# Performance work log

Measured on AMD Instinct MI355X. Metric: run time of the kernel, lower is better.

Reference implementation:

```python
import jax, jax.numpy as jnp
import numpy as np

D_K = 64


def setup_inputs() -> dict:
    key = jax.random.key(0)
    kq, kk, kv = jax.random.split(key, 3)
    B, H, S, D = 4, 16, 2048, 64
    return {
        "query": jax.random.normal(kq, (B, H, S, D), dtype=jnp.float32),
        "key": jax.random.normal(kk, (B, H, S, D), dtype=jnp.float32),
        "value": jax.random.normal(kv, (B, H, S, D), dtype=jnp.float32),
        "to_mask": 1,
    }


def reference(query, key, value, to_mask):
    # QK^T / sqrt(d_k): [B,H,S,S]
    scores = jnp.einsum("bhqd,bhkd->bhqk", query, key) / jnp.sqrt(
        jnp.asarray(D_K, dtype=query.dtype)
    )
    if to_mask:
        S = scores.shape[-1]
        # upper-triangular (strictly above diagonal) gets large negative bias
        causal = jnp.triu(jnp.ones((S, S), dtype=scores.dtype), k=1)
        scores = scores + causal[None, None, :, :] * jnp.asarray(-1e19, scores.dtype)
    attn = jax.nn.softmax(scores, axis=-1)
    return jnp.einsum("bhqk,bhkd->bhqd", attn, value)
```

## Files before the change

kernel.cpp:

```cpp
#include <hip/hip_runtime.h>
#include <math.h>

#define S_LEN 2048
#define D_HEAD 64
#define NT 32
#define BM 128
#define BN 64
#define TILE_HALFS 4096
#define PSTRIDE 72
#define QSCALE (0.125f * 1.44269504088896340736f)

typedef _Float16 f16;
typedef f16 f16x4 __attribute__((ext_vector_type(4)));
typedef f16 f16x8 __attribute__((ext_vector_type(8)));
typedef float f32x4 __attribute__((ext_vector_type(4)));

#define ASYNC16(g, l)                                                          \
    __builtin_amdgcn_global_load_lds(                                          \
        (const __attribute__((address_space(1))) void*)(g),                    \
        (__attribute__((address_space(3))) void*)(l), 16, 0, 0)

__global__ __launch_bounds__(256)
void prepass_kernel(const float* __restrict__ K, const float* __restrict__ V,
                    f16* __restrict__ Kw, f16* __restrict__ Vw) {
    const int kt = blockIdx.x, bh = blockIdx.y, tid = threadIdx.x;
    const int t = tid >> 6, lane = tid & 63, c = lane & 15, quad = lane >> 4;
    const size_t gbase = (size_t)bh * S_LEN * D_HEAD + (size_t)kt * BN * D_HEAD;
    const size_t tb = ((size_t)bh * NT + kt) * TILE_HALFS;

    __shared__ float Kt_s[64][65];
    __shared__ float Vt_s[64][65];

    float4 kv[4], vv[4];
    #pragma unroll
    for (int i = 0; i < 4; ++i) {
        const int fi = tid + i * 256;
        const int row = fi >> 4, d0 = (fi & 15) * 4;
        kv[i] = *(const float4*)(K + gbase + row * 64 + d0);
        vv[i] = *(const float4*)(V + gbase + row * 64 + d0);
    }
    #pragma unroll
    for (int i = 0; i < 4; ++i) {
        const int fi = tid + i * 256;
        const int row = fi >> 4, d0 = (fi & 15) * 4;
        Kt_s[row][d0 + 0] = kv[i].x; Kt_s[row][d0 + 1] = kv[i].y;
        Kt_s[row][d0 + 2] = kv[i].z; Kt_s[row][d0 + 3] = kv[i].w;
        Vt_s[row][d0 + 0] = vv[i].x; Vt_s[row][d0 + 1] = vv[i].y;
        Vt_s[row][d0 + 2] = vv[i].z; Vt_s[row][d0 + 3] = vv[i].w;
    }
    __syncthreads();

    #pragma unroll
    for (int ch = 0; ch < 2; ++ch) {
        const float* src = &Kt_s[t * 16 + c][ch * 32 + quad * 8];
        f16 h[8];
        #pragma unroll
        for (int j = 0; j < 8; ++j) h[j] = (f16)src[j];
        *(f16x8*)&Kw[tb + (size_t)((t * 2 + ch) * 64 + lane) * 8] = *(f16x8*)h;
    }
    #pragma unroll
    for (int ch = 0; ch < 2; ++ch) {
        f16 h[8];
        #pragma unroll
        for (int j = 0; j < 8; ++j)
            h[j] = (f16)Vt_s[ch * 32 + quad * 8 + j][t * 16 + c];
        *(f16x8*)&Vw[tb + (size_t)((t * 2 + ch) * 64 + lane) * 8] = *(f16x8*)h;
    }
}

__global__ __launch_bounds__(256, 3)
void fa_fwd_kernel(const float* __restrict__ Q, const f16* __restrict__ Kw,
                   const f16* __restrict__ Vw, const int* __restrict__ to_mask,
                   float* __restrict__ O) {
    const int qt   = (int)gridDim.x - 1 - (int)blockIdx.x;
    const int bh   = blockIdx.y;
    const int tid  = threadIdx.x;
    const int wave = tid >> 6;
    const int lane = tid & 63;
    const int c    = lane & 15;
    const int quad = lane >> 4;
    const int i0   = qt * BM;
    const int wrow0 = i0 + wave * 32;

    const int mask_on = to_mask[0];
    const int kt_end  = mask_on ? (2 * qt + 1) : (NT - 1);

    __shared__ __align__(16) f16 KV[2][2][TILE_HALFS];
    __shared__ __align__(16) f16 Ps[BM][PSTRIDE];

    const size_t base  = (size_t)bh * S_LEN * D_HEAD;
    const size_t tbase = (size_t)bh * NT * TILE_HALFS;

    f16x8 aq[2][2];
    #pragma unroll
    for (int set = 0; set < 2; ++set) {
        const float* qp = Q + base + (size_t)(wrow0 + set * 16 + c) * D_HEAD + quad * 8;
        #pragma unroll
        for (int ch = 0; ch < 2; ++ch) {
            const float4 a = *(const float4*)(qp + ch * 32);
            const float4 b = *(const float4*)(qp + ch * 32 + 4);
            aq[set][ch][0] = (f16)(a.x * QSCALE); aq[set][ch][1] = (f16)(a.y * QSCALE);
            aq[set][ch][2] = (f16)(a.z * QSCALE); aq[set][ch][3] = (f16)(a.w * QSCALE);
            aq[set][ch][4] = (f16)(b.x * QSCALE); aq[set][ch][5] = (f16)(b.y * QSCALE);
            aq[set][ch][6] = (f16)(b.z * QSCALE); aq[set][ch][7] = (f16)(b.w * QSCALE);
        }
    }

    f32x4 o[2][4];
    f32x4 accl[2];
    #pragma unroll
    for (int set = 0; set < 2; ++set) {
        accl[set] = (f32x4){0.f, 0.f, 0.f, 0.f};
        #pragma unroll
        for (int nt = 0; nt < 4; ++nt) o[set][nt] = (f32x4){0.f, 0.f, 0.f, 0.f};
    }

    const f16 one1 = (f16)1.0f;
    const f16x8 ones = {one1, one1, one1, one1, one1, one1, one1, one1};

    #pragma unroll
    for (int i = 0; i < 2; ++i) {
        const int s = wave * 2 + i;
        ASYNC16(Kw + tbase + s * 512 + lane * 8, &KV[0][0][s * 512]);
        ASYNC16(Vw + tbase + s * 512 + lane * 8, &KV[0][1][s * 512]);
    }

    for (int kt = 0; kt <= kt_end; ++kt) {
        __syncthreads();

        if (kt < kt_end) {
            const size_t tb = tbase + (size_t)(kt + 1) * TILE_HALFS;
            f16* lk = &KV[(kt + 1) & 1][0][0];
            f16* lv = &KV[(kt + 1) & 1][1][0];
            #pragma unroll
            for (int i = 0; i < 2; ++i) {
                const int s = wave * 2 + i;
                ASYNC16(Kw + tb + s * 512 + lane * 8, lk + s * 512);
                ASYNC16(Vw + tb + s * 512 + lane * 8, lv + s * 512);
            }
        }

        const int j0 = kt * BN;
        if (mask_on && j0 > wrow0 + 31) continue;

        const f16* Kt = &KV[kt & 1][0][0];
        const f16* Vv = &KV[kt & 1][1][0];

        f32x4 s[2][4];
        #pragma unroll
        for (int t = 0; t < 4; ++t) {
            const f16x8 kf0 = *(const f16x8*)&Kt[(t * 2 + 0) * 512 + lane * 8];
            const f16x8 kf1 = *(const f16x8*)&Kt[(t * 2 + 1) * 512 + lane * 8];
            #pragma unroll
            for (int set = 0; set < 2; ++set) {
                f32x4 acc = (f32x4){0.f, 0.f, 0.f, 0.f};
                acc = __builtin_amdgcn_mfma_f32_16x16x32_f16(kf0, aq[set][0], acc, 0, 0, 0);
                acc = __builtin_amdgcn_mfma_f32_16x16x32_f16(kf1, aq[set][1], acc, 0, 0, 0);
                s[set][t] = acc;
            }
        }

        if (mask_on && j0 + 63 > wrow0) {
            #pragma unroll
            for (int set = 0; set < 2; ++set)
                #pragma unroll
                for (int t = 0; t < 4; ++t)
                    #pragma unroll
                    for (int r = 0; r < 4; ++r)
                        if (j0 + t * 16 + quad * 4 + r > wrow0 + set * 16 + c)
                            s[set][t][r] = -1e30f;
        }

        #pragma unroll
        for (int set = 0; set < 2; ++set)
            #pragma unroll
            for (int t2 = 0; t2 < 4; ++t2) {
                f16x4 p;
                #pragma unroll
                for (int r = 0; r < 4; ++r)
                    p[r] = (f16)__builtin_amdgcn_exp2f(fminf(s[set][t2][r], 15.0f));
                *(f16x4*)&Ps[wave * 32 + set * 16 + c][t2 * 16 + quad * 4] = p;
            }

        f16x8 ap[2][2];
        #pragma unroll
        for (int set = 0; set < 2; ++set) {
            ap[set][0] = *(const f16x8*)&Ps[wave * 32 + set * 16 + c][quad * 8];
            ap[set][1] = *(const f16x8*)&Ps[wave * 32 + set * 16 + c][32 + quad * 8];
        }

        #pragma unroll
        for (int set = 0; set < 2; ++set) {
            accl[set] = __builtin_amdgcn_mfma_f32_16x16x32_f16(ap[set][0], ones, accl[set], 0, 0, 0);
            accl[set] = __builtin_amdgcn_mfma_f32_16x16x32_f16(ap[set][1], ones, accl[set], 0, 0, 0);
        }

        #pragma unroll
        for (int nt = 0; nt < 4; ++nt) {
            const f16x8 bv0 = *(const f16x8*)&Vv[(nt * 2 + 0) * 512 + lane * 8];
            const f16x8 bv1 = *(const f16x8*)&Vv[(nt * 2 + 1) * 512 + lane * 8];
            #pragma unroll
            for (int set = 0; set < 2; ++set) {
                o[set][nt] = __builtin_amdgcn_mfma_f32_16x16x32_f16(ap[set][0], bv0, o[set][nt], 0, 0, 0);
                o[set][nt] = __builtin_amdgcn_mfma_f32_16x16x32_f16(ap[set][1], bv1, o[set][nt], 0, 0, 0);
            }
        }
    }

    #pragma unroll
    for (int set = 0; set < 2; ++set)
        #pragma unroll
        for (int r = 0; r < 4; ++r) {
            const float inv = 1.0f / accl[set][r];
            float* op = O + base + (size_t)(wrow0 + set * 16 + quad * 4 + r) * D_HEAD;
            #pragma unroll
            for (int nt = 0; nt < 4; ++nt)
                op[nt * 16 + c] = o[set][nt][r] * inv;
        }
}

__global__ __launch_bounds__(256)
void fa_fwd_fallback(const float* __restrict__ Q, const float* __restrict__ K,
                     const float* __restrict__ V, const int* __restrict__ to_mask,
                     float* __restrict__ O) {
    const int qt = blockIdx.x, bh = blockIdx.y, tid = threadIdx.x;
    const int wave = tid >> 6, lane = tid & 63, c = lane & 15, quad = lane >> 4;
    const int i0 = qt * 64;
    const int mask_on = to_mask[0];
    const int kt_end = mask_on ? qt : (NT - 1);
    __shared__ __align__(16) f16 Ks[64][PSTRIDE];
    __shared__ __align__(16) f16 Vs[64][PSTRIDE];
    __shared__ __align__(16) f16 Psf[64][PSTRIDE];
    const size_t base = (size_t)bh * S_LEN * D_HEAD;
    f16x8 aq[2];
    {
        const float* qp = Q + base + (size_t)(i0 + wave * 16 + c) * D_HEAD + quad * 8;
        for (int ch = 0; ch < 2; ++ch)
            for (int j = 0; j < 8; ++j) aq[ch][j] = (f16)(qp[ch * 32 + j] * 0.125f);
    }
    f32x4 o[4]; float m_run[4], l_run[4], alpha_r[4];
    for (int t = 0; t < 4; ++t) o[t] = (f32x4){0.f, 0.f, 0.f, 0.f};
    for (int r = 0; r < 4; ++r) { m_run[r] = -INFINITY; l_run[r] = 0.f; }
    for (int kt = 0; kt <= kt_end; ++kt) {
        const int j0 = kt * 64;
        __syncthreads();
        for (int i = 0; i < 4; ++i) {
            const int f = tid + i * 256, key = f >> 4, d = (f & 15) * 4;
            const float4 kv = *(const float4*)(K + base + (size_t)(j0 + key) * D_HEAD + d);
            Ks[key][d] = (f16)kv.x; Ks[key][d + 1] = (f16)kv.y;
            Ks[key][d + 2] = (f16)kv.z; Ks[key][d + 3] = (f16)kv.w;
            const float4 vv = *(const float4*)(V + base + (size_t)(j0 + key) * D_HEAD + d);
            Vs[d][key] = (f16)vv.x; Vs[d + 1][key] = (f16)vv.y;
            Vs[d + 2][key] = (f16)vv.z; Vs[d + 3][key] = (f16)vv.w;
        }
        __syncthreads();
        f32x4 s[4];
        for (int t = 0; t < 4; ++t) {
            f32x4 acc = (f32x4){0.f, 0.f, 0.f, 0.f};
            const f16x8 b0 = *(const f16x8*)&Ks[t * 16 + c][quad * 8];
            const f16x8 b1 = *(const f16x8*)&Ks[t * 16 + c][32 + quad * 8];
            acc = __builtin_amdgcn_mfma_f32_16x16x32_f16(aq[0], b0, acc, 0, 0, 0);
            acc = __builtin_amdgcn_mfma_f32_16x16x32_f16(aq[1], b1, acc, 0, 0, 0);
            s[t] = acc;
        }
        if (mask_on && kt == qt)
            for (int t = 0; t < 4; ++t)
                for (int r = 0; r < 4; ++r)
                    if (t * 16 + c > wave * 16 + quad * 4 + r) s[t][r] = -1e30f;
        for (int r = 0; r < 4; ++r) {
            float mx = fmaxf(fmaxf(s[0][r], s[1][r]), fmaxf(s[2][r], s[3][r]));
            mx = fmaxf(mx, __shfl_xor(mx, 1)); mx = fmaxf(mx, __shfl_xor(mx, 2));
            mx = fmaxf(mx, __shfl_xor(mx, 4)); mx = fmaxf(mx, __shfl_xor(mx, 8));
            const float m_new = fmaxf(m_run[r], mx);
            const float alpha = __expf(m_run[r] - m_new);
            m_run[r] = m_new;
            float rs = 0.f;
            for (int t = 0; t < 4; ++t) { const float p = __expf(s[t][r] - m_new); s[t][r] = p; rs += p; }
            rs += __shfl_xor(rs, 1); rs += __shfl_xor(rs, 2);
            rs += __shfl_xor(rs, 4); rs += __shfl_xor(rs, 8);
            l_run[r] = l_run[r] * alpha + rs; alpha_r[r] = alpha;
        }
        for (int t = 0; t < 4; ++t)
            for (int r = 0; r < 4; ++r)
                Psf[wave * 16 + quad * 4 + r][t * 16 + c] = (f16)s[t][r];
        __syncthreads();
        const f16x8 ap0 = *(const f16x8*)&Psf[wave * 16 + c][quad * 8];
        const f16x8 ap1 = *(const f16x8*)&Psf[wave * 16 + c][32 + quad * 8];
        for (int t = 0; t < 4; ++t) {
            f32x4 acc = o[t];
            for (int r = 0; r < 4; ++r) acc[r] *= alpha_r[r];
            const f16x8 bv0 = *(const f16x8*)&Vs[t * 16 + c][quad * 8];
            const f16x8 bv1 = *(const f16x8*)&Vs[t * 16 + c][32 + quad * 8];
            acc = __builtin_amdgcn_mfma_f32_16x16x32_f16(ap0, bv0, acc, 0, 0, 0);
            acc = __builtin_amdgcn_mfma_f32_16x16x32_f16(ap1, bv1, acc, 0, 0, 0);
            o[t] = acc;
        }
    }
    for (int r = 0; r < 4; ++r) {
        const float inv = 1.f / l_run[r];
        float* op = O + base + (size_t)(i0 + wave * 16 + quad * 4 + r) * D_HEAD;
        for (int t = 0; t < 4; ++t) op[t * 16 + c] = o[t][r] * inv;
    }
}

extern "C" void kernel_launch(void* const* d_in, const int* in_sizes, int n_in,
                              void* d_out, int out_size, void* d_ws, size_t ws_size,
                              hipStream_t stream) {
    const float* Q = (const float*)d_in[0];
    const float* K = (const float*)d_in[1];
    const float* V = (const float*)d_in[2];
    const int* to_mask = (const int*)d_in[3];
    float* O = (float*)d_out;

    const size_t half_elems = (size_t)64 * S_LEN * D_HEAD;
    if (ws_size >= 2 * half_elems * sizeof(f16)) {
        f16* Kw = (f16*)d_ws;
        f16* Vw = Kw + half_elems;
        prepass_kernel<<<dim3(NT, 64), dim3(256), 0, stream>>>(K, V, Kw, Vw);
        fa_fwd_kernel<<<dim3(S_LEN / BM, 64), dim3(256), 0, stream>>>(Q, Kw, Vw, to_mask, O);
    } else {
        fa_fwd_fallback<<<dim3(NT, 64), dim3(256), 0, stream>>>(Q, K, V, to_mask, O);
    }
}
```

Measured before the change: 220.9 us.

## Triple-buffer K/V tiles with vmcnt waits, remap grid, and simplify K prepass

The attention kernel moves from double to triple buffering of the K/V LDS tiles, prefetching two tiles ahead. The per-iteration __syncthreads is replaced by a partial vmcnt wait plus a raw barrier, so loads stay in flight across iterations. Blocks are relaunched on a 1D grid whose index is remapped to interleave heads within each causal q-tile group, likely for L2 locality and load balance. The prepass now converts K straight from global memory without an LDS round trip. The larger LDS footprint lowers the occupancy hint from 3 to 2 blocks, and the hand-written waitcnt logic adds correctness risk.

Result: faster. 184.0 us (-16.7%).

```diff
diff --git a/kernel.cpp b/kernel.cpp
--- a/kernel.cpp
+++ b/kernel.cpp
@@ -6,6 +6,7 @@
 #define NT 32
 #define BM 128
 #define BN 64
+#define NQT (S_LEN / BM)
 #define TILE_HALFS 4096
 #define PSTRIDE 72
 #define QSCALE (0.125f * 1.44269504088896340736f)
@@ -28,36 +29,35 @@
     const size_t gbase = (size_t)bh * S_LEN * D_HEAD + (size_t)kt * BN * D_HEAD;
     const size_t tb = ((size_t)bh * NT + kt) * TILE_HALFS;
 
-    __shared__ float Kt_s[64][65];
     __shared__ float Vt_s[64][65];
 
-    float4 kv[4], vv[4];
+    float4 vv[4];
     #pragma unroll
     for (int i = 0; i < 4; ++i) {
         const int fi = tid + i * 256;
         const int row = fi >> 4, d0 = (fi & 15) * 4;
-        kv[i] = *(const float4*)(K + gbase + row * 64 + d0);
         vv[i] = *(const float4*)(V + gbase + row * 64 + d0);
     }
+
+    #pragma unroll
+    for (int ch = 0; ch < 2; ++ch) {
+        const float* src = K + gbase + (size_t)(t * 16 + c) * 64 + ch * 32 + quad * 8;
+        const float4 a = *(const float4*)src;
+        const float4 b = *(const float4*)(src + 4);
+        f16 h[8];
+        h[0] = (f16)a.x; h[1] = (f16)a.y; h[2] = (f16)a.z; h[3] = (f16)a.w;
+        h[4] = (f16)b.x; h[5] = (f16)b.y; h[6] = (f16)b.z; h[7] = (f16)b.w;
+        *(f16x8*)&Kw[tb + (size_t)((t * 2 + ch) * 64 + lane) * 8] = *(f16x8*)h;
+    }
+
     #pragma unroll
     for (int i = 0; i < 4; ++i) {
         const int fi = tid + i * 256;
         const int row = fi >> 4, d0 = (fi & 15) * 4;
-        Kt_s[row][d0 + 0] = kv[i].x; Kt_s[row][d0 + 1] = kv[i].y;
-        Kt_s[row][d0 + 2] = kv[i].z; Kt_s[row][d0 + 3] = kv[i].w;
         Vt_s[row][d0 + 0] = vv[i].x; Vt_s[row][d0 + 1] = vv[i].y;
         Vt_s[row][d0 + 2] = vv[i].z; Vt_s[row][d0 + 3] = vv[i].w;
     }
     __syncthreads();
-
-    #pragma unroll
-    for (int ch = 0; ch < 2; ++ch) {
-        const float* src = &Kt_s[t * 16 + c][ch * 32 + quad * 8];
-        f16 h[8];
-        #pragma unroll
-        for (int j = 0; j < 8; ++j) h[j] = (f16)src[j];
-        *(f16x8*)&Kw[tb + (size_t)((t * 2 + ch) * 64 + lane) * 8] = *(f16x8*)h;
-    }
     #pragma unroll
     for (int ch = 0; ch < 2; ++ch) {
         f16 h[8];
@@ -68,12 +68,15 @@
     }
 }
 
-__global__ __launch_bounds__(256, 3)
+__global__ __launch_bounds__(256, 2)
 void fa_fwd_kernel(const float* __restrict__ Q, const f16* __restrict__ Kw,
                    const f16* __restrict__ Vw, const int* __restrict__ to_mask,
                    float* __restrict__ O) {
-    const int qt   = (int)gridDim.x - 1 - (int)blockIdx.x;
-    const int bh   = blockIdx.y;
+    const int linear = (int)blockIdx.x;
+    const int g      = linear >> 3;
+    const int qt     = (NQT - 1) - (g >> 3);
+    const int bh     = (linear & 7) + 8 * (g & 7);
+
     const int tid  = threadIdx.x;
     const int wave = tid >> 6;
     const int lane = tid & 63;
@@ -85,7 +88,7 @@
     const int mask_on = to_mask[0];
     const int kt_end  = mask_on ? (2 * qt + 1) : (NT - 1);
 
-    __shared__ __align__(16) f16 KV[2][2][TILE_HALFS];
+    __shared__ __align__(16) f16 KV[3][2][TILE_HALFS];
     __shared__ __align__(16) f16 Ps[BM][PSTRIDE];
 
     const size_t base  = (size_t)bh * S_LEN * D_HEAD;
@@ -118,20 +121,31 @@
     const f16 one1 = (f16)1.0f;
     const f16x8 ones = {one1, one1, one1, one1, one1, one1, one1, one1};
 
+    asm volatile("s_waitcnt vmcnt(0)" ::: "memory");
+
     #pragma unroll
     for (int i = 0; i < 2; ++i) {
         const int s = wave * 2 + i;
         ASYNC16(Kw + tbase + s * 512 + lane * 8, &KV[0][0][s * 512]);
         ASYNC16(Vw + tbase + s * 512 + lane * 8, &KV[0][1][s * 512]);
     }
+    #pragma unroll
+    for (int i = 0; i < 2; ++i) {
+        const int s = wave * 2 + i;
+        ASYNC16(Kw + tbase + TILE_HALFS + s * 512 + lane * 8, &KV[1][0][s * 512]);
+        ASYNC16(Vw + tbase + TILE_HALFS + s * 512 + lane * 8, &KV[1][1][s * 512]);
+    }
 
     for (int kt = 0; kt <= kt_end; ++kt) {
-        __syncthreads();
-
-        if (kt < kt_end) {
-            const size_t tb = tbase + (size_t)(kt + 1) * TILE_HALFS;
-            f16* lk = &KV[(kt + 1) & 1][0][0];
-            f16* lv = &KV[(kt + 1) & 1][1][0];
+        asm volatile("s_waitcnt vmcnt(4)" ::: "memory");
+        __builtin_amdgcn_s_barrier();
+        __builtin_amdgcn_sched_barrier(0);
+
+        {
+            const int pf = (kt + 2 <= kt_end) ? (kt + 2) : kt_end;
+            const size_t tb = tbase + (size_t)pf * TILE_HALFS;
+            f16* lk = &KV[(kt + 2) % 3][0][0];
+            f16* lv = &KV[(kt + 2) % 3][1][0];
             #pragma unroll
             for (int i = 0; i < 2; ++i) {
                 const int s = wave * 2 + i;
@@ -143,8 +157,8 @@
         const int j0 = kt * BN;
         if (mask_on && j0 > wrow0 + 31) continue;
 
-        const f16* Kt = &KV[kt & 1][0][0];
-        const f16* Vv = &KV[kt & 1][1][0];
+        const f16* Kt = &KV[kt % 3][0][0];
+        const f16* Vv = &KV[kt % 3][1][0];
 
         f32x4 s[2][4];
         #pragma unroll
@@ -317,7 +331,7 @@
         f16* Kw = (f16*)d_ws;
         f16* Vw = Kw + half_elems;
         prepass_kernel<<<dim3(NT, 64), dim3(256), 0, stream>>>(K, V, Kw, Vw);
-        fa_fwd_kernel<<<dim3(S_LEN / BM, 64), dim3(256), 0, stream>>>(Q, Kw, Vw, to_mask, O);
+        fa_fwd_kernel<<<dim3(NQT * 64), dim3(256), 0, stream>>>(Q, Kw, Vw, to_mask, O);
     } else {
         fa_fwd_fallback<<<dim3(NT, 64), dim3(256), 0, stream>>>(Q, K, V, to_mask, O);
     }
```
